# Optimization experiments

Hardware: AMD Instinct MI355X
Metric: run time of the kernel (lower is better)

The kernel has to match this reference:

```python
import jax, jax.numpy as jnp
import numpy as np

NUM_HEADS = 12
DROP = 0.5


def setup_inputs() -> dict:
    key = jax.random.key(0)
    k1, k2, k3, k4 = jax.random.split(key, 4)
    B, N, C = 64, 577, 768
    x = jax.random.normal(k1, (B, N, C), dtype=jnp.float32)
    mask = jax.random.uniform(k2, (B, NUM_HEADS, N - 1), dtype=jnp.float32)
    Wqkv = jax.random.normal(k3, (C, 3 * C), dtype=jnp.float32) * 0.02
    bqkv = jnp.zeros((3 * C,), dtype=jnp.float32)
    Wproj = jax.random.normal(k4, (C, C), dtype=jnp.float32) * 0.02
    bproj = jnp.zeros((C,), dtype=jnp.float32)
    return {"x": x, "mask": mask, "Wqkv": Wqkv, "bqkv": bqkv,
            "Wproj": Wproj, "bproj": bproj}


def _drop_tokens(t, idx):
    # t: [B,H,N,D]; keep CLS token, gather sorted random indices from the rest
    rest = jnp.take_along_axis(t[:, :, 1:, :], idx[..., None], axis=2)
    return jnp.concatenate([t[:, :, :1, :], rest], axis=2)


def reference(x, mask, Wqkv, bqkv, Wproj, bproj):
    B, N, C = x.shape
    H = NUM_HEADS
    D = C // H
    scale = D ** -0.5
    target_len = N - int(N * DROP)  # kept tokens incl. CLS

    qkv = (x @ Wqkv + bqkv).reshape(B, N, 3, H, D)
    qkv = jnp.transpose(qkv, (2, 0, 3, 1, 4))  # [3,B,H,N,D]
    q, k, v = qkv[0], qkv[1], qkv[2]

    # random token drop (rand branch): topk of random mask, sort indices
    _, idx = jax.lax.top_k(mask, target_len - 1)  # [B,H,target_len-1]
    idx = jnp.sort(idx, axis=-1)
    k_p = _drop_tokens(k, idx)  # [B,H,target_len,D]
    v_p = _drop_tokens(v, idx)

    attn = jax.nn.softmax(
        jnp.einsum('bhnd,bhmd->bhnm', q, k_p) * scale, axis=-1)
    out = jnp.einsum('bhnm,bhmd->bhnd', attn, v_p)
    out = jnp.transpose(out, (0, 2, 1, 3)).reshape(B, N, C)
    return out @ Wproj + bproj
```

## Files before the change

### kernel.cpp

```cpp
#include <hip/hip_runtime.h>
#include <stdint.h>

#define B_      64
#define N_TOK   577
#define C_      768
#define H_      12
#define BH_     768
#define M_ROWS  36928
#define M_PAD   36992
#define KEEP    289
#define KP      320

typedef __attribute__((ext_vector_type(8))) short   bf16x8;
typedef __attribute__((ext_vector_type(4))) float   floatx4;
typedef __attribute__((ext_vector_type(4))) short   short4v;

static __device__ __forceinline__ unsigned short f2bf(float f) {
  union { float f; unsigned u; } a; a.f = f;
  unsigned u = a.u;
  u = u + 0x7FFFu + ((u >> 16) & 1u);
  return (unsigned short)(u >> 16);
}

static __device__ __forceinline__ void gl_lds16(const void* g, void* l) {
  __builtin_amdgcn_global_load_lds(
      (const __attribute__((address_space(1))) void*)g,
      (__attribute__((address_space(3))) void*)l, 16, 0, 0);
}

__global__ void topk_kernel(const float* __restrict__ mask, int* __restrict__ pos) {
  __shared__ float vals[576];
  __shared__ int woff[9];
  int row = blockIdx.x;
  int t = threadIdx.x;
  float v = mask[(size_t)row * 576 + t];
  vals[t] = v;
  __syncthreads();
  int rank = 0;
  for (int j = 0; j < 576; ++j) {
    float u = vals[j];
    rank += ((u > v) || (u == v && j < t)) ? 1 : 0;
  }
  bool sel = rank < (KEEP - 1);
  unsigned long long ball = __ballot(sel ? 1 : 0);
  int lane = t & 63, w = t >> 6;
  int lp = __popcll(ball & ((1ull << lane) - 1ull));
  if (lane == 0) woff[w] = __popcll(ball);
  __syncthreads();
  int base = 0;
  for (int i = 0; i < w; ++i) base += woff[i];
  pos[(size_t)row * 577 + 1 + t] = sel ? (1 + base + lp) : -1;
  if (t == 0) pos[(size_t)row * 577] = 0;
}

__global__ void convx_kernel(const float* __restrict__ x, unsigned short* __restrict__ xb) {
  size_t i = ((size_t)blockIdx.x * 256 + threadIdx.x) * 4;
  short4v o;
  if (i < (size_t)M_ROWS * C_) {
    float4 v = *(const float4*)(x + i);
    o.x = (short)f2bf(v.x); o.y = (short)f2bf(v.y);
    o.z = (short)f2bf(v.z); o.w = (short)f2bf(v.w);
  } else {
    o.x = 0; o.y = 0; o.z = 0; o.w = 0;
  }
  *(short4v*)(xb + i) = o;
}

__global__ void convwT_kernel(const float* __restrict__ W, unsigned short* __restrict__ Wt,
                              int N) {
  __shared__ unsigned short tile[64 * 72];
  int n0 = blockIdx.x * 64, k0 = blockIdx.y * 64;
  int t = threadIdx.x;
  for (int p = 0; p < 4; ++p) {
    int s = p * 256 + t;
    int k = s >> 4, nc = s & 15;
    float4 v = *(const float4*)(W + (size_t)(k0 + k) * N + n0 + nc * 4);
    short4v o;
    o.x = (short)f2bf(v.x); o.y = (short)f2bf(v.y);
    o.z = (short)f2bf(v.z); o.w = (short)f2bf(v.w);
    *(short4v*)(tile + k * 72 + nc * 4) = o;
  }
  __syncthreads();
  for (int p = 0; p < 2; ++p) {
    int s = p * 256 + t;
    int n = s >> 3, kc = s & 7;
    bf16x8 o;
    for (int j = 0; j < 8; ++j) o[j] = (short)tile[(kc * 8 + j) * 72 + n];
    *(bf16x8*)(Wt + (size_t)(n0 + n) * 768 + k0 + kc * 8) = o;
  }
}

__global__ void zeropad_kernel(unsigned short* __restrict__ Kp, unsigned short* __restrict__ Vp) {
  size_t idx = (size_t)blockIdx.x * 256 + threadIdx.x;
  int bh = (int)(idx / (31 * 64));
  int rem = (int)(idx % (31 * 64));
  int r = KEEP + rem / 64, d = rem & 63;
  size_t o = ((size_t)bh * KP + r) * 64 + d;
  Kp[o] = 0; Vp[o] = 0;
}

static __device__ __forceinline__ void stage_half(const unsigned short* src,
                                                  unsigned short* lds, int tid) {
#pragma unroll
  for (int c = 0; c < 2; ++c) {
    int s = c * 256 + tid;
    int r = s >> 3, cs = s & 7;
    int gc = (cs ^ (r & 7)) << 3;
    gl_lds16(src + (size_t)r * 768 + gc, lds + s * 8);
  }
}

static __device__ __forceinline__ void gemm8_core(
    const unsigned short* __restrict__ A, const unsigned short* __restrict__ Bt,
    int m0, int n0, int tid, unsigned short* As, unsigned short* Bs,
    floatx4 (&acc)[4][4]) {
  const int lane = tid & 63, wv = tid >> 6;
  const int quad = lane >> 4, lcol = lane & 15;
  const int wm = wv & 1, wn = wv >> 1;
  const int swz = lcol & 7;

#define STG_A(kt, half) stage_half(A  + (size_t)(m0 + 64*(half)) * 768 + (kt)*64, \
                                   As + ((kt)&1)*8192 + (half)*4096, tid)
#define STG_B(kt, half) stage_half(Bt + (size_t)(n0 + 64*(half)) * 768 + (kt)*64, \
                                   Bs + ((kt)&1)*8192 + (half)*4096, tid)

  STG_A(0, 0); STG_A(0, 1); STG_B(0, 0); STG_B(0, 1);
  STG_A(1, 0); STG_A(1, 1); STG_B(1, 0);
  asm volatile("s_waitcnt vmcnt(6)" ::: "memory");
  __builtin_amdgcn_s_barrier();

  for (int t = 0; t < 12; ++t) {
    const unsigned short* Asl = As + (t & 1) * 8192;
    const unsigned short* Bsl = Bs + (t & 1) * 8192;

    bf16x8 af[4][2], bfr[4][2];
#pragma unroll
    for (int i = 0; i < 4; ++i)
#pragma unroll
      for (int ks = 0; ks < 2; ++ks) {
        int cc = ks * 4 + quad;
        af[i][ks]  = *(const bf16x8*)(Asl + (wm * 64 + i * 16 + lcol) * 64 + ((cc ^ swz) << 3));
        bfr[i][ks] = *(const bf16x8*)(Bsl + (wn * 64 + i * 16 + lcol) * 64 + ((cc ^ swz) << 3));
      }
    if (t + 1 < 12) STG_B(t + 1, 1);
    asm volatile("s_waitcnt lgkmcnt(0)" ::: "memory");
    __builtin_amdgcn_sched_barrier(0);
    __builtin_amdgcn_s_barrier();
    __builtin_amdgcn_s_setprio(1);
#pragma unroll
    for (int j = 0; j < 4; ++j)
#pragma unroll
      for (int ks = 0; ks < 2; ++ks)
        acc[0][j] = __builtin_amdgcn_mfma_f32_16x16x32_bf16(af[0][ks], bfr[j][ks], acc[0][j], 0, 0, 0);
    __builtin_amdgcn_s_setprio(0);
    __builtin_amdgcn_s_barrier();

#pragma unroll
    for (int p = 1; p < 4; ++p) {
      if (t + 2 < 12) {
        if (p == 1)      STG_A(t + 2, 0);
        else if (p == 2) STG_A(t + 2, 1);
        else             STG_B(t + 2, 0);
      }
      __builtin_amdgcn_s_barrier();
      __builtin_amdgcn_s_setprio(1);
#pragma unroll
      for (int j = 0; j < 4; ++j)
#pragma unroll
        for (int ks = 0; ks < 2; ++ks)
          acc[p][j] = __builtin_amdgcn_mfma_f32_16x16x32_bf16(af[p][ks], bfr[j][ks], acc[p][j], 0, 0, 0);
      __builtin_amdgcn_s_setprio(0);
      if (p == 3) {
        if (t < 10)       asm volatile("s_waitcnt vmcnt(6)" ::: "memory");
        else if (t == 10) asm volatile("s_waitcnt vmcnt(0)" ::: "memory");
      }
      __builtin_amdgcn_s_barrier();
    }
  }
#undef STG_A
#undef STG_B
}

__global__ __launch_bounds__(256) void qkv_gemm_kernel(
    const unsigned short* __restrict__ A, const unsigned short* __restrict__ Bt,
    const float* __restrict__ bias, const int* __restrict__ pos,
    unsigned short* __restrict__ Q, unsigned short* __restrict__ Kp,
    unsigned short* __restrict__ Vp) {
  __shared__ unsigned short As[2 * 8192];
  __shared__ unsigned short Bs[2 * 8192];
  const int tid = threadIdx.x;
  const int lane = tid & 63, wv = tid >> 6;
  const int quad = lane >> 4, lcol = lane & 15;
  const int wm = wv & 1, wn = wv >> 1;
  int sid = blockIdx.x;
  int m_t, n_t;
  if (sid < 5184) {
    int sb = sid / 48, r = sid % 48;
    int gm = sb % 36, gn = sb / 36;
    m_t = gm * 8 + (r & 7);
    n_t = gn * 6 + (r >> 3);
  } else { m_t = 288; n_t = sid - 5184; }
  const int m0 = m_t * 128, n0 = n_t * 128;

  floatx4 acc[4][4] = {};
  gemm8_core(A, Bt, m0, n0, tid, As, Bs, acc);

  const int nbase = n0 + wn * 64;
  const int which = nbase / 768;
  const int h = (nbase - which * 768) >> 6;
  float bv[4];
#pragma unroll
  for (int nt = 0; nt < 4; ++nt) bv[nt] = bias[nbase + nt * 16 + lcol];
#pragma unroll
  for (int mt = 0; mt < 4; ++mt) {
#pragma unroll
    for (int r = 0; r < 4; ++r) {
      int m = m0 + wm * 64 + mt * 16 + quad * 4 + r;
      if (m >= M_ROWS) continue;
      int b = m / 577, t = m - b * 577;
      int bh = b * 12 + h;
      if (which == 0) {
        size_t base = ((size_t)bh * 577 + t) * 64;
#pragma unroll
        for (int nt = 0; nt < 4; ++nt)
          Q[base + nt * 16 + lcol] = f2bf(acc[mt][nt][r] + bv[nt]);
      } else {
        int p = pos[(size_t)bh * 577 + t];
        if (p >= 0) {
          size_t base = ((size_t)bh * KP + p) * 64;
          if (which == 1) {
            int sw = p & 7;
#pragma unroll
            for (int nt = 0; nt < 4; ++nt) {
              int d = nt * 16 + lcol;
              int d2 = (d & 7) | (((d >> 3) ^ sw) << 3);
              Kp[base + d2] = f2bf(acc[mt][nt][r] + bv[nt]);
            }
          } else {
#pragma unroll
            for (int nt = 0; nt < 4; ++nt)
              Vp[base + nt * 16 + lcol] = f2bf(acc[mt][nt][r] + bv[nt]);
          }
        }
      }
    }
  }
}

__global__ void transv_kernel(const unsigned short* __restrict__ Vp,
                              unsigned short* __restrict__ VpT) {
  __shared__ unsigned short tile[64 * 72];
  int bh = blockIdx.y, p0 = blockIdx.x * 64;
  int t = threadIdx.x;
  for (int pp = 0; pp < 2; ++pp) {
    int s = pp * 256 + t;
    int p = s >> 3, dc = s & 7;
    bf16x8 v = *(const bf16x8*)(Vp + ((size_t)bh * KP + p0 + p) * 64 + dc * 8);
    *(bf16x8*)(tile + p * 72 + dc * 8) = v;
  }
  __syncthreads();
  for (int pp = 0; pp < 2; ++pp) {
    int s = pp * 256 + t;
    int d = s >> 3, pc = s & 7;
    bf16x8 o;
    for (int j = 0; j < 8; ++j) o[j] = (short)tile[(pc * 8 + j) * 72 + d];
    *(bf16x8*)(VpT + ((size_t)bh * 64 + d) * KP + p0 + pc * 8) = o;
  }
}

__global__ __launch_bounds__(256) void attn_kernel(
    const unsigned short* __restrict__ Q, const unsigned short* __restrict__ Kp,
    const unsigned short* __restrict__ VpT, unsigned short* __restrict__ attnout) {
  __shared__ unsigned short S[320 * 64];
  const int tid = threadIdx.x;
  const int lane = tid & 63, w = tid >> 6;
  const int quad = lane >> 4, lcol = lane & 15;
  const int g = blockIdx.x;
  const int chunk = g / 80, within = g - chunk * 80;
  const int by = chunk * 8 + (within & 7);
  const int bx = within >> 3;
  const int q0 = bx * 64 + w * 16;

  const unsigned short* kg = Kp + (size_t)by * KP * 64;
#pragma unroll
  for (int c = 0; c < 10; ++c) {
    int s = c * 256 + tid;
    gl_lds16(kg + s * 8, S + s * 8);
  }

  bf16x8 aq[2];
  {
    int qr = q0 + lcol;
    if (qr < N_TOK) {
      const unsigned short* qp = Q + ((size_t)by * N_TOK + qr) * 64;
      aq[0] = *(const bf16x8*)(qp + quad * 8);
      aq[1] = *(const bf16x8*)(qp + 32 + quad * 8);
    } else {
      bf16x8 z = {0, 0, 0, 0, 0, 0, 0, 0};
      aq[0] = z; aq[1] = z;
    }
  }
  __syncthreads();

  floatx4 sacc[20] = {};
  __builtin_amdgcn_s_setprio(1);
#pragma unroll
  for (int nt = 0; nt < 19; ++nt) {
    int r16 = nt * 16 + lcol;
    const unsigned short* kb = S + r16 * 64;
    int sw = r16 & 7;
    bf16x8 b0 = *(const bf16x8*)(kb + ((quad ^ sw) << 3));
    bf16x8 b1 = *(const bf16x8*)(kb + (((quad + 4) ^ sw) << 3));
    sacc[nt] = __builtin_amdgcn_mfma_f32_16x16x32_bf16(aq[0], b0, sacc[nt], 0, 0, 0);
    sacc[nt] = __builtin_amdgcn_mfma_f32_16x16x32_bf16(aq[1], b1, sacc[nt], 0, 0, 0);
  }
  __builtin_amdgcn_s_setprio(0);

  const float scale = 0.125f;
  float inva[4];
  for (int r = 0; r < 4; ++r) {
    float mx = -1e30f;
#pragma unroll
    for (int nt = 0; nt < 20; ++nt) {
      int n = nt * 16 + lcol;
      float s = sacc[nt][r] * scale;
      if (n < KEEP) mx = fmaxf(mx, s);
    }
    for (int off = 1; off < 16; off <<= 1) mx = fmaxf(mx, __shfl_xor(mx, off, 64));
    float sum = 0.f;
#pragma unroll
    for (int nt = 0; nt < 20; ++nt) {
      int n = nt * 16 + lcol;
      float e = (n < KEEP) ? __expf(sacc[nt][r] * scale - mx) : 0.f;
      sacc[nt][r] = e;
      sum += e;
    }
    for (int off = 1; off < 16; off <<= 1) sum += __shfl_xor(sum, off, 64);
    inva[r] = 1.f / sum;
  }
  __syncthreads();

#pragma unroll
  for (int r = 0; r < 4; ++r) {
    int rowl = w * 16 + quad * 4 + r;
    int swp = rowl & 7;
#pragma unroll
    for (int nt = 0; nt < 20; ++nt) {
      int n = nt * 16 + lcol;
      int u = n >> 3;
      int u2 = (u & 0x38) | ((u & 7) ^ swp);
      S[rowl * 320 + u2 * 8 + (n & 7)] = f2bf(sacc[nt][r] * inva[r]);
    }
  }
  __syncthreads();

  floatx4 oacc[4] = {};
  const int prow = w * 16 + lcol;
  const int psw = prow & 7;
  __builtin_amdgcn_s_setprio(1);
#pragma unroll
  for (int kc = 0; kc < 10; ++kc) {
    int u = kc * 4 + quad;
    int u2 = (u & 0x38) | ((u & 7) ^ psw);
    bf16x8 pa = *(const bf16x8*)(S + prow * 320 + u2 * 8);
#pragma unroll
    for (int nt = 0; nt < 4; ++nt) {
      bf16x8 vb = *(const bf16x8*)(VpT + ((size_t)by * 64 + nt * 16 + lcol) * KP + kc * 32 + quad * 8);
      oacc[nt] = __builtin_amdgcn_mfma_f32_16x16x32_bf16(pa, vb, oacc[nt], 0, 0, 0);
    }
  }
  __builtin_amdgcn_s_setprio(0);

  int b = by / H_, h = by - b * H_;
#pragma unroll
  for (int nt = 0; nt < 4; ++nt)
#pragma unroll
    for (int r = 0; r < 4; ++r) {
      int qr = bx * 64 + w * 16 + quad * 4 + r;
      if (qr < N_TOK)
        attnout[((size_t)(b * N_TOK + qr)) * C_ + h * 64 + nt * 16 + lcol] = f2bf(oacc[nt][r]);
    }
}

__global__ __launch_bounds__(256) void proj_gemm_kernel(
    const unsigned short* __restrict__ A, const unsigned short* __restrict__ Bt,
    const float* __restrict__ bias, float* __restrict__ out) {
  __shared__ unsigned short As[2 * 8192];
  __shared__ unsigned short Bs[2 * 8192];
  const int tid = threadIdx.x;
  const int lane = tid & 63, wv = tid >> 6;
  const int quad = lane >> 4, lcol = lane & 15;
  const int wm = wv & 1, wn = wv >> 1;
  int sid = blockIdx.x;
  int m_t, n_t;
  if (sid < 1728) {
    int sb = sid / 48, r = sid % 48;
    m_t = sb * 8 + (r & 7);
    n_t = r >> 3;
  } else { m_t = 288; n_t = sid - 1728; }
  const int m0 = m_t * 128, n0 = n_t * 128;

  floatx4 acc[4][4] = {};
  gemm8_core(A, Bt, m0, n0, tid, As, Bs, acc);

  const int nbase = n0 + wn * 64;
  float bv[4];
#pragma unroll
  for (int nt = 0; nt < 4; ++nt) bv[nt] = bias[nbase + nt * 16 + lcol];
#pragma unroll
  for (int mt = 0; mt < 4; ++mt)
#pragma unroll
    for (int r = 0; r < 4; ++r) {
      int m = m0 + wm * 64 + mt * 16 + quad * 4 + r;
      if (m >= M_ROWS) continue;
#pragma unroll
      for (int nt = 0; nt < 4; ++nt)
        out[(size_t)m * C_ + nbase + nt * 16 + lcol] = acc[mt][nt][r] + bv[nt];
    }
}

extern "C" void kernel_launch(void* const* d_in, const int* in_sizes, int n_in,
                              void* d_out, int out_size, void* d_ws, size_t ws_size,
                              hipStream_t stream) {
  const float* x     = (const float*)d_in[0];
  const float* mask  = (const float*)d_in[1];
  const float* Wqkv  = (const float*)d_in[2];
  const float* bqkv  = (const float*)d_in[3];
  const float* Wproj = (const float*)d_in[4];
  const float* bproj = (const float*)d_in[5];
  float* out = (float*)d_out;

  char* ws = (char*)d_ws;
  unsigned short* xb     = (unsigned short*)(ws);
  unsigned short* attno  = xb;
  unsigned short* WqkvT  = (unsigned short*)(ws + 56819712);
  unsigned short* WprojT = (unsigned short*)(ws + 60358656);
  int*            pos    = (int*)(ws + 61538304);
  unsigned short* Qb     = (unsigned short*)(ws + 63310848);
  unsigned short* Kpb    = (unsigned short*)(ws + 120032256);
  unsigned short* Vpb    = (unsigned short*)(ws + 151489536);
  unsigned short* VpTb   = (unsigned short*)(ws + 182946816);

  hipLaunchKernelGGL(topk_kernel,     dim3(768),      dim3(576), 0, stream, mask, pos);
  hipLaunchKernelGGL(convx_kernel,    dim3(27744),    dim3(256), 0, stream, x, xb);
  hipLaunchKernelGGL(convwT_kernel,   dim3(36, 12),   dim3(256), 0, stream, Wqkv, WqkvT, 2304);
  hipLaunchKernelGGL(convwT_kernel,   dim3(12, 12),   dim3(256), 0, stream, Wproj, WprojT, 768);
  hipLaunchKernelGGL(zeropad_kernel,  dim3(5952),     dim3(256), 0, stream, Kpb, Vpb);
  hipLaunchKernelGGL(qkv_gemm_kernel, dim3(5202),     dim3(256), 0, stream, xb, WqkvT, bqkv, pos, Qb, Kpb, Vpb);
  hipLaunchKernelGGL(transv_kernel,   dim3(5, 768),   dim3(256), 0, stream, Vpb, VpTb);
  hipLaunchKernelGGL(attn_kernel,     dim3(7680),     dim3(256), 0, stream, Qb, Kpb, VpTb, attno);
  hipLaunchKernelGGL(proj_gemm_kernel,dim3(1734),     dim3(256), 0, stream, attno, WprojT, bproj, out);
}
```

Measured before the change: 686.3 us.

## Stage V tile in LDS asynchronously and overlap its load with QK^T

The attention kernel now issues async global-to-LDS loads for the transposed V tile right after the K tile, waiting only on the K loads before the QK^T phase so the V transfer overlaps with score computation and softmax. The PV loop then reads V from LDS instead of from global memory. To keep those LDS reads bank-conflict free, the transpose kernel writes VpT with an XOR swizzle that the PV loop undoes. The second block-wide barrier after the P writes is replaced by a local lgkmcnt wait, which relies on each wave reading back only its own P rows. Total LDS per block doubles to about 80 KB, which may reduce occupancy.

```diff
diff --git a/kernel.cpp b/kernel.cpp
--- a/kernel.cpp
+++ b/kernel.cpp
@@ -264,7 +264,8 @@
     int d = s >> 3, pc = s & 7;
     bf16x8 o;
     for (int j = 0; j < 8; ++j) o[j] = (short)tile[(pc * 8 + j) * 72 + d];
-    *(bf16x8*)(VpT + ((size_t)bh * 64 + d) * KP + p0 + pc * 8) = o;
+    int pc2 = pc ^ (d & 7);
+    *(bf16x8*)(VpT + ((size_t)bh * 64 + d) * KP + p0 + pc2 * 8) = o;
   }
 }
 
@@ -272,6 +273,7 @@
     const unsigned short* __restrict__ Q, const unsigned short* __restrict__ Kp,
     const unsigned short* __restrict__ VpT, unsigned short* __restrict__ attnout) {
   __shared__ unsigned short S[320 * 64];
+  __shared__ unsigned short Vs[64 * 320];
   const int tid = threadIdx.x;
   const int lane = tid & 63, w = tid >> 6;
   const int quad = lane >> 4, lcol = lane & 15;
@@ -280,13 +282,6 @@
   const int by = chunk * 8 + (within & 7);
   const int bx = within >> 3;
   const int q0 = bx * 64 + w * 16;
-
-  const unsigned short* kg = Kp + (size_t)by * KP * 64;
-#pragma unroll
-  for (int c = 0; c < 10; ++c) {
-    int s = c * 256 + tid;
-    gl_lds16(kg + s * 8, S + s * 8);
-  }
 
   bf16x8 aq[2];
   {
@@ -300,7 +295,26 @@
       aq[0] = z; aq[1] = z;
     }
   }
-  __syncthreads();
+  __builtin_amdgcn_sched_barrier(0);
+
+  const unsigned short* kg = Kp + (size_t)by * KP * 64;
+#pragma unroll
+  for (int c = 0; c < 10; ++c) {
+    int s = c * 256 + tid;
+    gl_lds16(kg + s * 8, S + s * 8);
+  }
+  __builtin_amdgcn_sched_barrier(0);
+  const unsigned short* vg = VpT + (size_t)by * 64 * KP;
+#pragma unroll
+  for (int c = 0; c < 10; ++c) {
+    int s = c * 256 + tid;
+    gl_lds16(vg + s * 8, Vs + s * 8);
+  }
+  __builtin_amdgcn_sched_barrier(0);
+
+  asm volatile("s_waitcnt vmcnt(10)" ::: "memory");
+  __builtin_amdgcn_sched_barrier(0);
+  __builtin_amdgcn_s_barrier();
 
   floatx4 sacc[20] = {};
   __builtin_amdgcn_s_setprio(1);
@@ -338,7 +352,10 @@
     for (int off = 1; off < 16; off <<= 1) sum += __shfl_xor(sum, off, 64);
     inva[r] = 1.f / sum;
   }
-  __syncthreads();
+
+  asm volatile("s_waitcnt lgkmcnt(0) vmcnt(0)" ::: "memory");
+  __builtin_amdgcn_sched_barrier(0);
+  __builtin_amdgcn_s_barrier();
 
 #pragma unroll
   for (int r = 0; r < 4; ++r) {
@@ -352,20 +369,23 @@
       S[rowl * 320 + u2 * 8 + (n & 7)] = f2bf(sacc[nt][r] * inva[r]);
     }
   }
-  __syncthreads();
+  asm volatile("s_waitcnt lgkmcnt(0)" ::: "memory");
+  __builtin_amdgcn_sched_barrier(0);
 
   floatx4 oacc[4] = {};
   const int prow = w * 16 + lcol;
   const int psw = prow & 7;
+  const int vsw = lcol & 7;
   __builtin_amdgcn_s_setprio(1);
 #pragma unroll
   for (int kc = 0; kc < 10; ++kc) {
     int u = kc * 4 + quad;
-    int u2 = (u & 0x38) | ((u & 7) ^ psw);
-    bf16x8 pa = *(const bf16x8*)(S + prow * 320 + u2 * 8);
+    int pu2 = (u & 0x38) | ((u & 7) ^ psw);
+    bf16x8 pa = *(const bf16x8*)(S + prow * 320 + pu2 * 8);
+    int vu2 = (u & 0x38) | ((u & 7) ^ vsw);
 #pragma unroll
     for (int nt = 0; nt < 4; ++nt) {
-      bf16x8 vb = *(const bf16x8*)(VpT + ((size_t)by * 64 + nt * 16 + lcol) * KP + kc * 32 + quad * 8);
+      bf16x8 vb = *(const bf16x8*)(Vs + (nt * 16 + lcol) * 320 + vu2 * 8);
       oacc[nt] = __builtin_amdgcn_mfma_f32_16x16x32_bf16(pa, vb, oacc[nt], 0, 0, 0);
     }
   }
```

Measured after the change: 595.4 us. 13.2% less time.
